# Kernel optimization log

Hardware: AMD Instinct MI355X
Metric: run time of the kernel (lower is better)

Reference implementation:

```python
import jax, jax.numpy as jnp
import numpy as np

N_NODES = 100000


def gcn_conv(x, edge_index, W, b, n_nodes):
    # PyG GCNConv: x' = D^{-1/2} (A + I) D^{-1/2} (x W) + b
    src, dst = edge_index[0], edge_index[1]
    h = x @ W  # linear transform first (in_ch >= out_ch path in PyG)
    # degree with self-loops, computed on target nodes
    deg = jax.ops.segment_sum(jnp.ones_like(dst, dtype=h.dtype), dst,
                              num_segments=n_nodes) + 1.0
    dinv = jax.lax.rsqrt(deg)  # deg >= 1 due to self-loops
    # edge messages: norm_e * h[src]
    norm_e = dinv[src] * dinv[dst]  # [E]
    msg = h[src] * norm_e[:, None]  # [E, out]
    agg = jax.ops.segment_sum(msg, dst, num_segments=n_nodes)
    # self-loop contribution: dinv[i]^2 * h[i]
    out = agg + h * (dinv * dinv)[:, None] + b
    return out


def setup_inputs() -> dict:
    key = jax.random.key(0)
    k1, k2, k3, k4 = jax.random.split(key, 4)
    N, E, F, H, C = N_NODES, 1600000, 128, 64, 32
    x = jax.random.normal(k1, (N, F), dtype=jnp.float32)
    edge_index = jax.random.randint(k2, (2, E), 0, N, dtype=jnp.int64)
    # glorot-style init
    W1 = jax.random.normal(k3, (F, H), dtype=jnp.float32) * (1.0 / np.sqrt(F))
    W2 = jax.random.normal(k4, (H, C), dtype=jnp.float32) * (1.0 / np.sqrt(H))
    b1 = jnp.zeros((H,), dtype=jnp.float32)
    b2 = jnp.zeros((C,), dtype=jnp.float32)
    return {"x": x, "edge_index": edge_index, "W1": W1, "b1": b1,
            "W2": W2, "b2": b2}


def reference(x, edge_index, W1, b1, W2, b2):
    n = x.shape[0]
    h = gcn_conv(x, edge_index, W1, b1, n)
    h = jax.nn.relu(h)
    # dropout is identity in eval mode (reference baseline)
    out = gcn_conv(h, edge_index, W2, b2, n)
    return out
```

## Files before the change

kernel.cpp:

```cpp
#include <hip/hip_runtime.h>
#include <hip/hip_fp16.h>

#define B_HIST 512
#define SHIFT  9

typedef _Float16 f16x8 __attribute__((ext_vector_type(8)));
typedef float f32x4 __attribute__((ext_vector_type(4)));
typedef float f32x2 __attribute__((ext_vector_type(2)));

#define FP8_SCALE 32.0f
#define FP8_INV   (1.0f / 32.0f)


__global__ __launch_bounds__(256) void p1_hist(const int* __restrict__ dst,
                                               int* __restrict__ histT, int E) {
  __shared__ int h[256];
  const int t = threadIdx.x;
  h[t] = 0;
  __syncthreads();
  const int epb = (E + B_HIST - 1) / B_HIST;
  const int beg = blockIdx.x * epb;
  const int end = min(beg + epb, E);
  for (int e = beg + t; e < end; e += 256)
    atomicAdd(&h[dst[e] >> SHIFT], 1);
  __syncthreads();
  histT[t * B_HIST + blockIdx.x] = h[t];
}

__global__ __launch_bounds__(256) void p2a_colscan(int* __restrict__ histT,
                                                   int* __restrict__ bsum) {
  __shared__ int sdata[256];
  const int bin = blockIdx.x, t = threadIdx.x;
  const int i0 = bin * B_HIST + 2 * t;
  int c0 = histT[i0], c1 = histT[i0 + 1];
  int s = c0 + c1;
  sdata[t] = s;
  __syncthreads();
  for (int off = 1; off < 256; off <<= 1) {
    int x = 0;
    if (t >= off) x = sdata[t - off];
    __syncthreads();
    if (t >= off) sdata[t] += x;
    __syncthreads();
  }
  int excl = sdata[t] - s;
  histT[i0] = excl;
  histT[i0 + 1] = excl + c0;
  if (t == 255) bsum[bin] = sdata[255];
}

__global__ __launch_bounds__(256) void p2b_scan(const int* __restrict__ bsum,
                                                int* __restrict__ colstart) {
  __shared__ int sdata[256];
  const int t = threadIdx.x;
  int v = bsum[t];
  sdata[t] = v;
  __syncthreads();
  for (int off = 1; off < 256; off <<= 1) {
    int x = 0;
    if (t >= off) x = sdata[t - off];
    __syncthreads();
    if (t >= off) sdata[t] += x;
    __syncthreads();
  }
  colstart[t] = sdata[t] - v;
  if (t == 255) colstart[256] = sdata[255];
}

__global__ __launch_bounds__(256) void p3_scatter(const int* __restrict__ src,
                                                  const int* __restrict__ dst,
                                                  const int* __restrict__ histT,
                                                  const int* __restrict__ colstart,
                                                  int* __restrict__ pbuf, int E) {
  __shared__ int cur[256];
  const int t = threadIdx.x;
  cur[t] = colstart[t] + histT[t * B_HIST + blockIdx.x];
  __syncthreads();
  const int epb = (E + B_HIST - 1) / B_HIST;
  const int beg = blockIdx.x * epb;
  const int end = min(beg + epb, E);
  for (int e = beg + t; e < end; e += 256) {
    int d = dst[e];
    int s = src[e];
    int pos = atomicAdd(&cur[d >> SHIFT], 1);
    pbuf[pos] = ((d & 511) << 17) | s;
  }
}

__global__ __launch_bounds__(256) void p4_fine(const int* __restrict__ pbuf,
                                               const int* __restrict__ colstart,
                                               int* __restrict__ rowptr,
                                               float* __restrict__ dinv,
                                               int* __restrict__ ssrc, int N, int NB) {
  __shared__ int cnt[512];
  __shared__ int sdata[256];
  __shared__ int cur[512];
  const int b = blockIdx.x, t = threadIdx.x;
  const int base = colstart[b], endp = colstart[b + 1];
  cnt[2 * t] = 0; cnt[2 * t + 1] = 0;
  __syncthreads();
  for (int i = base + t; i < endp; i += 256)
    atomicAdd(&cnt[pbuf[i] >> 17], 1);
  __syncthreads();
  int c0 = cnt[2 * t], c1 = cnt[2 * t + 1];
  int s = c0 + c1;
  sdata[t] = s;
  __syncthreads();
  for (int off = 1; off < 256; off <<= 1) {
    int x = 0;
    if (t >= off) x = sdata[t - off];
    __syncthreads();
    if (t >= off) sdata[t] += x;
    __syncthreads();
  }
  int excl = sdata[t] - s;
  int e0 = base + excl, e1 = base + excl + c0;
  cur[2 * t] = e0;
  cur[2 * t + 1] = e1;
  int node0 = (b << SHIFT) + 2 * t;
  if (node0 < N) {
    rowptr[node0] = e0;
    dinv[node0] = rsqrtf((float)c0 + 1.0f);
  }
  if (node0 + 1 < N) {
    rowptr[node0 + 1] = e1;
    dinv[node0 + 1] = rsqrtf((float)c1 + 1.0f);
  }
  if (b == NB - 1 && t == 0) rowptr[N] = endp;
  __syncthreads();
  for (int i = base + t; i < endp; i += 256) {
    int p = pbuf[i];
    int pos = atomicAdd(&cur[p >> 17], 1);
    ssrc[pos] = p & 0x1FFFF;
  }
}


template <int COLS, int K>
__global__ __launch_bounds__(256) void wpack_kernel(const float* __restrict__ W,
                                                    _Float16* __restrict__ P) {
  int task = blockIdx.x * 256 + threadIdx.x;
  if (task >= (K / 8) * COLS) return;
  int col = task % COLS;
  int kq = task / COLS;
  _Float16 tmp[8];
#pragma unroll
  for (int j = 0; j < 8; ++j)
    tmp[j] = (_Float16)W[(kq * 8 + j) * COLS + col];
  *reinterpret_cast<f16x8*>(&P[task * 8]) = *reinterpret_cast<const f16x8*>(tmp);
}


template <int COLS, int K, typename XT, bool FP8_OUT>
__global__ __launch_bounds__(256) void mfma_gemm(const XT* __restrict__ X,
                                                 const _Float16* __restrict__ wpk,
                                                 const float* __restrict__ dinv,
                                                 void* __restrict__ O, int N) {
  constexpr int NKK = K / 32;
  constexpr int NCT = COLS / 16;
  constexpr int RCH = K / 8;
  constexpr int SWM = RCH - 1;
  __shared__ _Float16 xs[64 * K];
  __shared__ _Float16 wb[K * COLS];
  const int t = threadIdx.x;
  const int row0 = blockIdx.x * 64;

  for (int i = t; i < K * COLS / 8; i += 256)
    *reinterpret_cast<f16x8*>(&wb[i * 8]) = reinterpret_cast<const f16x8*>(wpk)[i];
  for (int task = t; task < 64 * RCH; task += 256) {
    int row = task / RCH, c = task % RCH;
    int grow = row0 + row;
    f16x8 hv;
#pragma unroll
    for (int j = 0; j < 8; ++j) hv[j] = (_Float16)0.f;
    if (grow < N) {
      if constexpr (sizeof(XT) == 4) {
        const float4* xr = reinterpret_cast<const float4*>(X + (size_t)grow * K);
        float4 v0 = xr[c * 2], v1 = xr[c * 2 + 1];
        hv[0] = (_Float16)v0.x; hv[1] = (_Float16)v0.y;
        hv[2] = (_Float16)v0.z; hv[3] = (_Float16)v0.w;
        hv[4] = (_Float16)v1.x; hv[5] = (_Float16)v1.y;
        hv[6] = (_Float16)v1.z; hv[7] = (_Float16)v1.w;
      } else {
        hv = reinterpret_cast<const f16x8*>(X + (size_t)grow * K)[c];
      }
    }
    int sc = c ^ (row & SWM);
    *reinterpret_cast<f16x8*>(&xs[row * K + sc * 8]) = hv;
  }
  __syncthreads();

  const int wave = t >> 6, lane = t & 63;
  const int q = lane >> 4, c = lane & 15;
  const int wrow = wave * 16;

  f16x8 bfrag[NKK][NCT];
#pragma unroll
  for (int kk = 0; kk < NKK; ++kk)
#pragma unroll
    for (int ct = 0; ct < NCT; ++ct)
      bfrag[kk][ct] = *reinterpret_cast<const f16x8*>(
          &wb[(size_t)((kk * 4 + q) * COLS + ct * 16 + c) * 8]);

  f32x4 acc[NCT];
#pragma unroll
  for (int ct = 0; ct < NCT; ++ct) acc[ct] = {0.f, 0.f, 0.f, 0.f};

#pragma unroll
  for (int kk = 0; kk < NKK; ++kk) {
    int row = wrow + c;
    int cc = (kk * 4 + q) ^ (row & SWM);
    f16x8 afrag = *reinterpret_cast<const f16x8*>(&xs[row * K + cc * 8]);
#pragma unroll
    for (int ct = 0; ct < NCT; ++ct)
      acc[ct] = __builtin_amdgcn_mfma_f32_16x16x32_f16(afrag, bfrag[kk][ct], acc[ct], 0, 0, 0);
  }

#pragma unroll
  for (int r = 0; r < 4; ++r) {
    int row = row0 + wrow + q * 4 + r;
    if (row < N) {
      float di = dinv[row];
#pragma unroll
      for (int ct = 0; ct < NCT; ++ct) {
        int col = ct * 16 + c;
        if constexpr (FP8_OUT) {
          float v = acc[ct][r] * di * FP8_SCALE;
          int pk = __builtin_amdgcn_cvt_pk_fp8_f32(v, v, 0, false);
          ((unsigned char*)O)[(size_t)row * COLS + col] = (unsigned char)(pk & 0xFF);
        } else {
          ((__half*)O)[(size_t)row * COLS + col] = __float2half(acc[ct][r] * di);
        }
      }
    }
  }
}

__global__ __launch_bounds__(256) void gather64_fp8_kernel(const int* __restrict__ rowptr,
                                                           const int* __restrict__ ssrc,
                                                           const float* __restrict__ dinv,
                                                           const unsigned int* __restrict__ g8,
                                                           const float4* __restrict__ bias,
                                                           __half* __restrict__ outb, int N) {
  int node = (blockIdx.x * 256 + threadIdx.x) >> 4;
  int col = threadIdx.x & 15;
  if (node >= N) return;
  int beg = rowptr[node], end = rowptr[node + 1];
  float4 aa0 = {0.f, 0.f, 0.f, 0.f}, aa1 = aa0, aa2 = aa0, aa3 = aa0;
  for (int base = beg; base < end; base += 16) {
    int m = end - base;
    int sv = 0;
    if (col < m) sv = ssrc[base + col];
    unsigned int v[16];
#pragma unroll
    for (int u = 0; u < 16; ++u) {
      if (u < m) {
        int s = __shfl(sv, u, 16);
        v[u] = g8[(size_t)s * 16 + col];
      }
    }
#pragma unroll
    for (int u = 0; u < 16; ++u) {
      if (u < m) {
        f32x2 lo = __builtin_amdgcn_cvt_pk_f32_fp8((int)v[u], false);
        f32x2 hi = __builtin_amdgcn_cvt_pk_f32_fp8((int)v[u], true);
        if ((u & 3) == 0) { aa0.x += lo.x; aa0.y += lo.y; aa0.z += hi.x; aa0.w += hi.y; }
        if ((u & 3) == 1) { aa1.x += lo.x; aa1.y += lo.y; aa1.z += hi.x; aa1.w += hi.y; }
        if ((u & 3) == 2) { aa2.x += lo.x; aa2.y += lo.y; aa2.z += hi.x; aa2.w += hi.y; }
        if ((u & 3) == 3) { aa3.x += lo.x; aa3.y += lo.y; aa3.z += hi.x; aa3.w += hi.y; }
      }
    }
  }
  unsigned int vs = g8[(size_t)node * 16 + col];
  f32x2 slo = __builtin_amdgcn_cvt_pk_f32_fp8((int)vs, false);
  f32x2 shi = __builtin_amdgcn_cvt_pk_f32_fp8((int)vs, true);
  float inv = dinv[node] * FP8_INV;
  float4 bb = bias[col];
  float ox = fmaxf(fmaf(inv, (aa0.x + aa1.x) + (aa2.x + aa3.x) + slo.x, bb.x), 0.f);
  float oy = fmaxf(fmaf(inv, (aa0.y + aa1.y) + (aa2.y + aa3.y) + slo.y, bb.y), 0.f);
  float oz = fmaxf(fmaf(inv, (aa0.z + aa1.z) + (aa2.z + aa3.z) + shi.x, bb.z), 0.f);
  float ow = fmaxf(fmaf(inv, (aa0.w + aa1.w) + (aa2.w + aa3.w) + shi.y, bb.w), 0.f);
  union { __half2 h2[2]; uint2 u; } cv;
  cv.h2[0] = __floats2half2_rn(ox, oy);
  cv.h2[1] = __floats2half2_rn(oz, ow);
  reinterpret_cast<uint2*>(outb)[(size_t)node * 16 + col] = cv.u;
}

__global__ __launch_bounds__(256) void gather32_kernel(const int* __restrict__ rowptr,
                                                       const int* __restrict__ ssrc,
                                                       const float* __restrict__ dinv,
                                                       const uint2* __restrict__ g,
                                                       const float4* __restrict__ bias,
                                                       float4* __restrict__ outb, int N) {
  int node = (blockIdx.x * 256 + threadIdx.x) >> 3;
  int col = threadIdx.x & 7;
  if (node >= N) return;
  int beg = rowptr[node], end = rowptr[node + 1];
  float4 aa0 = {0.f, 0.f, 0.f, 0.f}, aa1 = aa0, aa2 = aa0, aa3 = aa0;
  for (int base = beg; base < end; base += 16) {
    int m = end - base;
    int sv0 = 0, sv1 = 0;
    if (col < m) sv0 = ssrc[base + col];
    if (col + 8 < m) sv1 = ssrc[base + 8 + col];
    uint2 v[16];
#pragma unroll
    for (int u = 0; u < 8; ++u) {
      if (u < m) {
        int s = __shfl(sv0, u, 8);
        v[u] = g[(size_t)s * 8 + col];
      }
    }
#pragma unroll
    for (int u = 8; u < 16; ++u) {
      if (u < m) {
        int s = __shfl(sv1, u - 8, 8);
        v[u] = g[(size_t)s * 8 + col];
      }
    }
#pragma unroll
    for (int u = 0; u < 16; ++u) {
      if (u < m) {
        float2 f0 = __half22float2(*(__half2*)&v[u].x);
        float2 f1 = __half22float2(*(__half2*)&v[u].y);
        if ((u & 3) == 0) { aa0.x += f0.x; aa0.y += f0.y; aa0.z += f1.x; aa0.w += f1.y; }
        if ((u & 3) == 1) { aa1.x += f0.x; aa1.y += f0.y; aa1.z += f1.x; aa1.w += f1.y; }
        if ((u & 3) == 2) { aa2.x += f0.x; aa2.y += f0.y; aa2.z += f1.x; aa2.w += f1.y; }
        if ((u & 3) == 3) { aa3.x += f0.x; aa3.y += f0.y; aa3.z += f1.x; aa3.w += f1.y; }
      }
    }
  }
  uint2 vs = g[(size_t)node * 8 + col];
  float2 g01 = __half22float2(*(__half2*)&vs.x);
  float2 g23 = __half22float2(*(__half2*)&vs.y);
  float di = dinv[node];
  float4 bb = bias[col];
  float4 o;
  o.x = fmaf(di, (aa0.x + aa1.x) + (aa2.x + aa3.x) + g01.x, bb.x);
  o.y = fmaf(di, (aa0.y + aa1.y) + (aa2.y + aa3.y) + g01.y, bb.y);
  o.z = fmaf(di, (aa0.z + aa1.z) + (aa2.z + aa3.z) + g23.x, bb.z);
  o.w = fmaf(di, (aa0.w + aa1.w) + (aa2.w + aa3.w) + g23.y, bb.w);
  outb[(size_t)node * 8 + col] = o;
}


extern "C" void kernel_launch(void* const* d_in, const int* in_sizes, int n_in,
                              void* d_out, int out_size, void* d_ws, size_t ws_size,
                              hipStream_t stream) {
  const float* x  = (const float*)d_in[0];
  const int*   ei = (const int*)d_in[1];
  const float* W1 = (const float*)d_in[2];
  const float* b1 = (const float*)d_in[3];
  const float* W2 = (const float*)d_in[4];
  const float* b2 = (const float*)d_in[5];
  float* out = (float*)d_out;

  const int H = in_sizes[3];
  const int F = in_sizes[2] / H;
  const int N = in_sizes[0] / F;
  const int E = in_sizes[1] / 2;
  const int* src = ei;
  const int* dst = ei + E;
  const int NB = (N + 511) >> SHIFT;

  char* w = (char*)d_ws;
  auto alloc = [&](size_t bytes) { char* p = w; w += (bytes + 255) & ~(size_t)255; return p; };
  int*           histT    = (int*)alloc((size_t)256 * B_HIST * 4);
  int*           bsum     = (int*)alloc(256 * 4);
  int*           colstart = (int*)alloc(257 * 4);
  int*           pbuf     = (int*)alloc((size_t)E * 4);
  int*           ssrc     = (int*)alloc((size_t)E * 4);
  int*           rowptr   = (int*)alloc((size_t)(N + 1) * 4);
  float*         dinv     = (float*)alloc((size_t)N * 4);
  _Float16*      wp1      = (_Float16*)alloc((size_t)128 * 64 * 2);
  _Float16*      wp2      = (_Float16*)alloc((size_t)64 * 32 * 2);
  unsigned char* g1q      = (unsigned char*)alloc((size_t)N * 64);
  __half*        buf1     = (__half*)alloc((size_t)N * 64 * 2);
  __half*        g2       = (__half*)alloc((size_t)N * 32 * 2);

  wpack_kernel<64, 128><<<4, 256, 0, stream>>>(W1, wp1);
  wpack_kernel<32, 64><<<1, 256, 0, stream>>>(W2, wp2);

  p1_hist<<<B_HIST, 256, 0, stream>>>(dst, histT, E);
  p2a_colscan<<<256, 256, 0, stream>>>(histT, bsum);
  p2b_scan<<<1, 256, 0, stream>>>(bsum, colstart);
  p3_scatter<<<B_HIST, 256, 0, stream>>>(src, dst, histT, colstart, pbuf, E);
  p4_fine<<<NB, 256, 0, stream>>>(pbuf, colstart, rowptr, dinv, ssrc, N, NB);

  mfma_gemm<64, 128, float, true><<<(N + 63) / 64, 256, 0, stream>>>(x, wp1, dinv, g1q, N);
  gather64_fp8_kernel<<<(N * 16 + 255) / 256, 256, 0, stream>>>(rowptr, ssrc, dinv,
      (const unsigned int*)g1q, (const float4*)b1, buf1, N);

  mfma_gemm<32, 64, _Float16, false><<<(N + 63) / 64, 256, 0, stream>>>(
      (const _Float16*)buf1, wp2, dinv, g2, N);
  gather32_kernel<<<(N * 8 + 255) / 256, 256, 0, stream>>>(rowptr, ssrc, dinv,
      (const uint2*)g2, (const float4*)b2, (float4*)out, N);
}
```

Measured before the change: 141.7 us.

## Split gathered feature tables into column panels and gather each panel separately

The GEMM outputs are written in a column-panel layout (two 32-byte fp8 panels for layer 1, two 32-byte fp16 panels for layer 2). Each gather then runs twice, once per panel, with narrower per-node rows. The goal is to shrink the working set of each random-gather pass so the table stays more cache resident (each panel is about 3.2 MB). The cost is reading rowptr and ssrc twice, extra launches, and narrower 4-byte loads per lane.

```diff
diff --git a/kernel.cpp b/kernel.cpp
--- a/kernel.cpp
+++ b/kernel.cpp
@@ -227,38 +227,41 @@
         if constexpr (FP8_OUT) {
           float v = acc[ct][r] * di * FP8_SCALE;
           int pk = __builtin_amdgcn_cvt_pk_fp8_f32(v, v, 0, false);
-          ((unsigned char*)O)[(size_t)row * COLS + col] = (unsigned char)(pk & 0xFF);
+          ((unsigned char*)O)[(size_t)(col >> 5) * N * 32 + (size_t)row * 32 + (col & 31)] =
+              (unsigned char)(pk & 0xFF);
         } else {
-          ((__half*)O)[(size_t)row * COLS + col] = __float2half(acc[ct][r] * di);
+          ((__half*)O)[(size_t)(col >> 4) * N * 16 + (size_t)row * 16 + (col & 15)] =
+              __float2half(acc[ct][r] * di);
         }
       }
     }
   }
 }
 
-__global__ __launch_bounds__(256) void gather64_fp8_kernel(const int* __restrict__ rowptr,
-                                                           const int* __restrict__ ssrc,
-                                                           const float* __restrict__ dinv,
-                                                           const unsigned int* __restrict__ g8,
-                                                           const float4* __restrict__ bias,
-                                                           __half* __restrict__ outb, int N) {
-  int node = (blockIdx.x * 256 + threadIdx.x) >> 4;
-  int col = threadIdx.x & 15;
+__global__ __launch_bounds__(256) void gather64p_kernel(const int* __restrict__ rowptr,
+                                                        const int* __restrict__ ssrc,
+                                                        const float* __restrict__ dinv,
+                                                        const unsigned int* __restrict__ gh,
+                                                        const float* __restrict__ bias32,
+                                                        __half* __restrict__ outb,
+                                                        int colbase, int N) {
+  int node = (blockIdx.x * 256 + threadIdx.x) >> 3;
+  int col = threadIdx.x & 7;
   if (node >= N) return;
   int beg = rowptr[node], end = rowptr[node + 1];
   float4 aa0 = {0.f, 0.f, 0.f, 0.f}, aa1 = aa0, aa2 = aa0, aa3 = aa0;
   for (int base = beg; base < end; base += 16) {
     int m = end - base;
-    int sv = 0;
-    if (col < m) sv = ssrc[base + col];
+    int sv0 = 0, sv1 = 0;
+    if (col < m) sv0 = ssrc[base + col];
+    if (col + 8 < m) sv1 = ssrc[base + 8 + col];
     unsigned int v[16];
 #pragma unroll
-    for (int u = 0; u < 16; ++u) {
-      if (u < m) {
-        int s = __shfl(sv, u, 16);
-        v[u] = g8[(size_t)s * 16 + col];
-      }
-    }
+    for (int u = 0; u < 8; ++u)
+      if (u < m) v[u] = gh[(size_t)__shfl(sv0, u, 8) * 8 + col];
+#pragma unroll
+    for (int u = 8; u < 16; ++u)
+      if (u < m) v[u] = gh[(size_t)__shfl(sv1, u - 8, 8) * 8 + col];
 #pragma unroll
     for (int u = 0; u < 16; ++u) {
       if (u < m) {
@@ -271,11 +274,11 @@
       }
     }
   }
-  unsigned int vs = g8[(size_t)node * 16 + col];
+  unsigned int vs = gh[(size_t)node * 8 + col];
   f32x2 slo = __builtin_amdgcn_cvt_pk_f32_fp8((int)vs, false);
   f32x2 shi = __builtin_amdgcn_cvt_pk_f32_fp8((int)vs, true);
   float inv = dinv[node] * FP8_INV;
-  float4 bb = bias[col];
+  float4 bb = *reinterpret_cast<const float4*>(bias32 + 4 * col);
   float ox = fmaxf(fmaf(inv, (aa0.x + aa1.x) + (aa2.x + aa3.x) + slo.x, bb.x), 0.f);
   float oy = fmaxf(fmaf(inv, (aa0.y + aa1.y) + (aa2.y + aa3.y) + slo.y, bb.y), 0.f);
   float oz = fmaxf(fmaf(inv, (aa0.z + aa1.z) + (aa2.z + aa3.z) + shi.x, bb.z), 0.f);
@@ -283,63 +286,52 @@
   union { __half2 h2[2]; uint2 u; } cv;
   cv.h2[0] = __floats2half2_rn(ox, oy);
   cv.h2[1] = __floats2half2_rn(oz, ow);
-  reinterpret_cast<uint2*>(outb)[(size_t)node * 16 + col] = cv.u;
-}
-
-__global__ __launch_bounds__(256) void gather32_kernel(const int* __restrict__ rowptr,
-                                                       const int* __restrict__ ssrc,
-                                                       const float* __restrict__ dinv,
-                                                       const uint2* __restrict__ g,
-                                                       const float4* __restrict__ bias,
-                                                       float4* __restrict__ outb, int N) {
+  *reinterpret_cast<uint2*>(outb + (size_t)node * 64 + colbase + 4 * col) = cv.u;
+}
+
+__global__ __launch_bounds__(256) void gather32p_kernel(const int* __restrict__ rowptr,
+                                                        const int* __restrict__ ssrc,
+                                                        const float* __restrict__ dinv,
+                                                        const unsigned int* __restrict__ gh,
+                                                        const float* __restrict__ bias16,
+                                                        float* __restrict__ outb,
+                                                        int colbase, int N) {
   int node = (blockIdx.x * 256 + threadIdx.x) >> 3;
   int col = threadIdx.x & 7;
   if (node >= N) return;
   int beg = rowptr[node], end = rowptr[node + 1];
-  float4 aa0 = {0.f, 0.f, 0.f, 0.f}, aa1 = aa0, aa2 = aa0, aa3 = aa0;
+  float2 aa0 = {0.f, 0.f}, aa1 = aa0, aa2 = aa0, aa3 = aa0;
   for (int base = beg; base < end; base += 16) {
     int m = end - base;
     int sv0 = 0, sv1 = 0;
     if (col < m) sv0 = ssrc[base + col];
     if (col + 8 < m) sv1 = ssrc[base + 8 + col];
-    uint2 v[16];
-#pragma unroll
-    for (int u = 0; u < 8; ++u) {
+    unsigned int v[16];
+#pragma unroll
+    for (int u = 0; u < 8; ++u)
+      if (u < m) v[u] = gh[(size_t)__shfl(sv0, u, 8) * 8 + col];
+#pragma unroll
+    for (int u = 8; u < 16; ++u)
+      if (u < m) v[u] = gh[(size_t)__shfl(sv1, u - 8, 8) * 8 + col];
+#pragma unroll
+    for (int u = 0; u < 16; ++u) {
       if (u < m) {
-        int s = __shfl(sv0, u, 8);
-        v[u] = g[(size_t)s * 8 + col];
+        float2 f = __half22float2(*(__half2*)&v[u]);
+        if ((u & 3) == 0) { aa0.x += f.x; aa0.y += f.y; }
+        if ((u & 3) == 1) { aa1.x += f.x; aa1.y += f.y; }
+        if ((u & 3) == 2) { aa2.x += f.x; aa2.y += f.y; }
+        if ((u & 3) == 3) { aa3.x += f.x; aa3.y += f.y; }
       }
     }
-#pragma unroll
-    for (int u = 8; u < 16; ++u) {
-      if (u < m) {
-        int s = __shfl(sv1, u - 8, 8);
-        v[u] = g[(size_t)s * 8 + col];
-      }
-    }
-#pragma unroll
-    for (int u = 0; u < 16; ++u) {
-      if (u < m) {
-        float2 f0 = __half22float2(*(__half2*)&v[u].x);
-        float2 f1 = __half22float2(*(__half2*)&v[u].y);
-        if ((u & 3) == 0) { aa0.x += f0.x; aa0.y += f0.y; aa0.z += f1.x; aa0.w += f1.y; }
-        if ((u & 3) == 1) { aa1.x += f0.x; aa1.y += f0.y; aa1.z += f1.x; aa1.w += f1.y; }
-        if ((u & 3) == 2) { aa2.x += f0.x; aa2.y += f0.y; aa2.z += f1.x; aa2.w += f1.y; }
-        if ((u & 3) == 3) { aa3.x += f0.x; aa3.y += f0.y; aa3.z += f1.x; aa3.w += f1.y; }
-      }
-    }
-  }
-  uint2 vs = g[(size_t)node * 8 + col];
-  float2 g01 = __half22float2(*(__half2*)&vs.x);
-  float2 g23 = __half22float2(*(__half2*)&vs.y);
+  }
+  unsigned int vs = gh[(size_t)node * 8 + col];
+  float2 gs = __half22float2(*(__half2*)&vs);
   float di = dinv[node];
-  float4 bb = bias[col];
-  float4 o;
-  o.x = fmaf(di, (aa0.x + aa1.x) + (aa2.x + aa3.x) + g01.x, bb.x);
-  o.y = fmaf(di, (aa0.y + aa1.y) + (aa2.y + aa3.y) + g01.y, bb.y);
-  o.z = fmaf(di, (aa0.z + aa1.z) + (aa2.z + aa3.z) + g23.x, bb.z);
-  o.w = fmaf(di, (aa0.w + aa1.w) + (aa2.w + aa3.w) + g23.y, bb.w);
-  outb[(size_t)node * 8 + col] = o;
+  float2 bb = *reinterpret_cast<const float2*>(bias16 + 2 * col);
+  float2 o;
+  o.x = fmaf(di, (aa0.x + aa1.x) + (aa2.x + aa3.x) + gs.x, bb.x);
+  o.y = fmaf(di, (aa0.y + aa1.y) + (aa2.y + aa3.y) + gs.y, bb.y);
+  *reinterpret_cast<float2*>(outb + (size_t)node * 32 + colbase + 2 * col) = o;
 }
 
 
@@ -386,12 +378,16 @@
   p3_scatter<<<B_HIST, 256, 0, stream>>>(src, dst, histT, colstart, pbuf, E);
   p4_fine<<<NB, 256, 0, stream>>>(pbuf, colstart, rowptr, dinv, ssrc, N, NB);
 
+  const int gblocks = (N * 8 + 255) / 256;
+
   mfma_gemm<64, 128, float, true><<<(N + 63) / 64, 256, 0, stream>>>(x, wp1, dinv, g1q, N);
-  gather64_fp8_kernel<<<(N * 16 + 255) / 256, 256, 0, stream>>>(rowptr, ssrc, dinv,
-      (const unsigned int*)g1q, (const float4*)b1, buf1, N);
+  for (int q = 0; q < 2; ++q)
+    gather64p_kernel<<<gblocks, 256, 0, stream>>>(rowptr, ssrc, dinv,
+        (const unsigned int*)(g1q + (size_t)q * N * 32), b1 + 32 * q, buf1, 32 * q, N);
 
   mfma_gemm<32, 64, _Float16, false><<<(N + 63) / 64, 256, 0, stream>>>(
       (const _Float16*)buf1, wp2, dinv, g2, N);
-  gather32_kernel<<<(N * 8 + 255) / 256, 256, 0, stream>>>(rowptr, ssrc, dinv,
-      (const uint2*)g2, (const float4*)b2, (float4*)out, N);
-}
+  for (int q = 0; q < 2; ++q)
+    gather32p_kernel<<<gblocks, 256, 0, stream>>>(rowptr, ssrc, dinv,
+        (const unsigned int*)g2 + (size_t)q * N * 8, b2 + 16 * q, out, 16 * q, N);
+}
```

After: 162.5 us. 1.15x slower.
